# Performance work log

Measured on AMD Instinct MI355X. Metric: run time of the kernel, lower is better.

## Reference

```python
import jax, jax.numpy as jnp
import numpy as np

B, T, F = 8, 8192, 512
FREQ = T // 2 + 1


def setup_inputs() -> dict:
    key = jax.random.key(0)
    k1, k2 = jax.random.split(key)
    x = jax.random.normal(k1, (B, T, F), dtype=jnp.float32)
    # learnable complex filter stored as [F, FREQ, 2] (real, imag)
    H = jax.random.normal(k2, (F, FREQ, 2), dtype=jnp.float32) * 0.1
    # identity-ish init like the module: real part centered at 1
    H = H.at[..., 0].add(1.0)
    return {"x": x, "H": H}


def reference(x, H):
    # X: [B, FREQ, F] complex
    X = jnp.fft.rfft(x, axis=1, norm="ortho")
    Hc = (H[..., 0] + 1j * H[..., 1]).T  # [FREQ, F]
    Y = X * Hc[None, :, :]
    y = jnp.fft.irfft(Y, n=T, axis=1, norm="ortho")  # [B, T, F] real
    return y
```

## Files before the change

kernel.cpp:

```cpp
#include <hip/hip_runtime.h>


#define THREADS 512
#define NFFT 8192
#define TT 8192
#define FFD2 256
#define FREQ 4097

#define IDX(i) ((i) + ((i) >> 5))
#define LDS_SZ (NFFT + NFFT / 32)

__device__ __forceinline__ float2 cmul(float2 a, float2 b) {
    return make_float2(a.x * b.x - a.y * b.y, a.x * b.y + a.y * b.x);
}

#define BF1(i0, i1) { float2 a = v[i0], b = v[i1]; \
    v[i0] = make_float2(a.x + b.x, a.y + b.y); \
    v[i1] = make_float2(a.x - b.x, a.y - b.y); }
#define BFI(i0, i1) { float2 a = v[i0], b = v[i1]; \
    v[i0] = make_float2(a.x + b.x, a.y + b.y); \
    float dr = a.x - b.x, di = a.y - b.y; \
    v[i1] = make_float2(-di * S, dr * S); }
#define BFW(i0, i1, wr, wi) { float2 a = v[i0], b = v[i1]; \
    v[i0] = make_float2(a.x + b.x, a.y + b.y); \
    float dr = a.x - b.x, di = a.y - b.y; \
    v[i1] = make_float2(dr * (wr) - di * (wi), dr * (wi) + di * (wr)); }

template<int SGN>
__device__ __forceinline__ void dft16(float2 v[16]) {
    constexpr float S  = (float)SGN;
    constexpr float RT = 0.70710678118654752440f;
    constexpr float C1 = 0.92387953251128675613f;
    constexpr float S1 = 0.38268343236508977173f;
    BF1(0, 8); BFW(1, 9, C1, S * S1); BFW(2, 10, RT, S * RT); BFW(3, 11, S1, S * C1);
    BFI(4, 12); BFW(5, 13, -S1, S * C1); BFW(6, 14, -RT, S * RT); BFW(7, 15, -C1, S * S1);
    BF1(0, 4); BFW(1, 5, RT, S * RT); BFI(2, 6); BFW(3, 7, -RT, S * RT);
    BF1(8, 12); BFW(9, 13, RT, S * RT); BFI(10, 14); BFW(11, 15, -RT, S * RT);
    BF1(0, 2); BFI(1, 3); BF1(4, 6); BFI(5, 7);
    BF1(8, 10); BFI(9, 11); BF1(12, 14); BFI(13, 15);
    BF1(0, 1); BF1(2, 3); BF1(4, 5); BF1(6, 7);
    BF1(8, 9); BF1(10, 11); BF1(12, 13); BF1(14, 15);
}

__global__ __launch_bounds__(THREADS, 4) void fft_filter_kernel(
    const float* __restrict__ x, const float* __restrict__ H,
    float* __restrict__ y)
{
    __shared__ float re[LDS_SZ];
    __shared__ float im[LDS_SZ];

    const int tid = threadIdx.x;
    const int wg = blockIdx.x;
    const int id = (wg & 7) * 256 + (wg >> 3);
    const int b  = id >> 8;
    const int j  = id & 255;

    const float2* __restrict__ xp = (const float2*)x;
    float2* __restrict__ yp = (float2*)y;
    const size_t base = (size_t)b * TT * FFD2 + j;

    constexpr int R4[16] = {0, 8, 4, 12, 2, 10, 6, 14, 1, 9, 5, 13, 3, 11, 7, 15};
    const float TWO_PI = 6.28318530717958647692f;

    float2 v[16];

    {
        const int r1 = tid;
#pragma unroll
        for (int t = 0; t < 16; ++t)
            v[t] = xp[base + (size_t)((t * 512 + r1) * FFD2)];
        dft16<-1>(v);
        float sn, cs;
        __sincosf(-TWO_PI * (float)r1 / 8192.0f, &sn, &cs);
        const float2 wb = make_float2(cs, sn);
        float2 w = make_float2(1.0f, 0.0f);
#pragma unroll
        for (int u = 0; u < 16; ++u) {
            const float2 val = (u == 0) ? v[0] : cmul(v[R4[u]], w);
            const int a = IDX(u * 512 + r1);
            re[a] = val.x; im[a] = val.y;
            w = cmul(w, wb);
        }
    }
    __syncthreads();

    {
        const int ub = tid >> 5, r2 = tid & 31;
        const int bb = ub * 512 + r2;
#pragma unroll
        for (int t = 0; t < 16; ++t) {
            const int a = IDX(bb + t * 32);
            v[t] = make_float2(re[a], im[a]);
        }
        dft16<-1>(v);
        float sn, cs;
        __sincosf(-TWO_PI * (float)r2 / 512.0f, &sn, &cs);
        const float2 wb = make_float2(cs, sn);
        float2 w = make_float2(1.0f, 0.0f);
#pragma unroll
        for (int u = 0; u < 16; ++u) {
            const float2 val = (u == 0) ? v[0] : cmul(v[R4[u]], w);
            const int a = IDX(bb + u * 32);
            re[a] = val.x; im[a] = val.y;
            w = cmul(w, wb);
        }
    }
    __syncthreads();

    {
        const int b3 = tid >> 1, r3 = tid & 1;
        const int bb = b3 * 32 + r3;
#pragma unroll
        for (int t = 0; t < 16; ++t) {
            const int a = IDX(bb + t * 2);
            v[t] = make_float2(re[a], im[a]);
        }
        dft16<-1>(v);
        float sn, cs;
        __sincosf(-TWO_PI * (float)r3 / 32.0f, &sn, &cs);
        const float2 wb = make_float2(cs, sn);
        float2 w = make_float2(1.0f, 0.0f);
#pragma unroll
        for (int u = 0; u < 16; ++u) {
            const float2 A = (u == 0) ? v[0] : cmul(v[R4[u]], w);
            float2 o;
            o.x = __shfl_xor(A.x, 1);
            o.y = __shfl_xor(A.y, 1);
            const float2 val = r3 ? make_float2(o.x - A.x, o.y - A.y)
                                  : make_float2(A.x + o.x, A.y + o.y);
            const int a = IDX(bb + u * 2);
            re[a] = val.x; im[a] = val.y;
            w = cmul(w, wb);
        }
    }
    __syncthreads();

    {
        const float2* __restrict__ Hp = (const float2*)H;
        const size_t hb0 = (size_t)(2 * j) * FREQ;
        const size_t hb1 = hb0 + FREQ;
        const float invN = 1.0f / 8192.0f;
#pragma unroll
        for (int q = 0; q < 16; ++q) {
            const int u = tid + q * THREADS;
            if (u == 0) {
                const int a = IDX(0);
                const float zr = re[a], zi = im[a];
                re[a] = zr * Hp[hb0].x * invN;
                im[a] = zi * Hp[hb1].x * invN;
            } else if (u == 1) {
                const int a = IDX(1);
                const float zr = re[a], zi = im[a];
                re[a] = zr * Hp[hb0 + 4096].x * invN;
                im[a] = zi * Hp[hb1 + 4096].x * invN;
            } else {
                const int k  = ((u >> 9) & 15) | (((u >> 5) & 15) << 4)
                             | (((u >> 1) & 15) << 8) | ((u & 1) << 12);
                const int k2 = NFFT - k;
                const int p2 = ((k2 & 15) << 9) | (((k2 >> 4) & 15) << 5)
                             | (((k2 >> 8) & 15) << 1) | ((k2 >> 12) & 1);
                if (u < p2) {
                    const bool swapd = (k > NFFT / 2);
                    const int klo = swapd ? k2 : k;
                    const int pz = swapd ? p2 : u;
                    const int pw = swapd ? u : p2;
                    const int az = IDX(pz), aw = IDX(pw);
                    const float z1r = re[az], z1i = im[az];
                    const float z2r = re[aw], z2i = im[aw];
                    const float xar = 0.5f * (z1r + z2r), xai = 0.5f * (z1i - z2i);
                    const float xbr = 0.5f * (z1i + z2i), xbi = 0.5f * (z2r - z1r);
                    const float2 ha  = Hp[hb0 + klo];
                    const float2 hbv = Hp[hb1 + klo];
                    const float har = ha.x * invN,  hai = ha.y * invN;
                    const float hbr = hbv.x * invN, hbi = hbv.y * invN;
                    const float yar = xar * har - xai * hai;
                    const float yai = xar * hai + xai * har;
                    const float ybr = xbr * hbr - xbi * hbi;
                    const float ybi = xbr * hbi + xbi * hbr;
                    re[az] = yar - ybi;
                    im[az] = yai + ybr;
                    re[aw] = yar + ybi;
                    im[aw] = ybr - yai;
                }
            }
        }
    }
    __syncthreads();

    {
        const int b3 = tid >> 1, r3 = tid & 1;
        const int bb = b3 * 32 + r3;
        float sn, cs;
        __sincosf(TWO_PI * (float)r3 / 32.0f, &sn, &cs);
        const float2 wb = make_float2(cs, sn);
        float2 w = make_float2(1.0f, 0.0f);
#pragma unroll
        for (int u = 0; u < 16; ++u) {
            const int a = IDX(bb + u * 2);
            const float2 o = make_float2(re[a], im[a]);
            float2 p;
            p.x = __shfl_xor(o.x, 1);
            p.y = __shfl_xor(o.y, 1);
            const float2 U = r3 ? make_float2(p.x - o.x, p.y - o.y)
                                : make_float2(o.x + p.x, o.y + p.y);
            v[u] = (u == 0) ? U : cmul(U, w);
            w = cmul(w, wb);
        }
        dft16<1>(v);
#pragma unroll
        for (int t = 0; t < 16; ++t) {
            const int a = IDX(bb + t * 2);
            re[a] = v[R4[t]].x; im[a] = v[R4[t]].y;
        }
    }
    __syncthreads();

    {
        const int ub = tid >> 5, r2 = tid & 31;
        const int bb = ub * 512 + r2;
        float sn, cs;
        __sincosf(TWO_PI * (float)r2 / 512.0f, &sn, &cs);
        const float2 wb = make_float2(cs, sn);
        float2 w = make_float2(1.0f, 0.0f);
#pragma unroll
        for (int u = 0; u < 16; ++u) {
            const int a = IDX(bb + u * 32);
            const float2 U = make_float2(re[a], im[a]);
            v[u] = (u == 0) ? U : cmul(U, w);
            w = cmul(w, wb);
        }
        dft16<1>(v);
#pragma unroll
        for (int t = 0; t < 16; ++t) {
            const int a = IDX(bb + t * 32);
            re[a] = v[R4[t]].x; im[a] = v[R4[t]].y;
        }
    }
    __syncthreads();

    {
        const int r1 = tid;
        float sn, cs;
        __sincosf(TWO_PI * (float)r1 / 8192.0f, &sn, &cs);
        const float2 wb = make_float2(cs, sn);
        float2 w = make_float2(1.0f, 0.0f);
#pragma unroll
        for (int u = 0; u < 16; ++u) {
            const int a = IDX(u * 512 + r1);
            const float2 U = make_float2(re[a], im[a]);
            v[u] = (u == 0) ? U : cmul(U, w);
            w = cmul(w, wb);
        }
        dft16<1>(v);
#pragma unroll
        for (int t = 0; t < 16; ++t)
            yp[base + (size_t)((t * 512 + r1) * FFD2)] = v[R4[t]];
    }
}

extern "C" void kernel_launch(void* const* d_in, const int* in_sizes, int n_in,
                              void* d_out, int out_size, void* d_ws, size_t ws_size,
                              hipStream_t stream) {
    const float* x = (const float*)d_in[0];
    const float* H = (const float*)d_in[1];
    float* y = (float*)d_out;
    fft_filter_kernel<<<dim3(2048), dim3(THREADS), 0, stream>>>(x, H, y);
}
```

Before: 419.3 us.

## Split fused FFT filter into three-kernel four-step FFT via workspace

Replaces the single fused kernel, where each workgroup ran a full 8192-point FFT in LDS, with three kernels. The first does a 64-point first-stage FFT with twiddles and writes to a global workspace. The second does 128-point FFTs plus the pointwise filter multiply, pairing conjugate-symmetric columns, and then the inverse 128-point stage. The third does the final inverse 64-point stage. The aim is to cut LDS use per block and raise occupancy and coalescing, at the cost of two extra full round trips of intermediate data through global memory.

```diff
diff --git a/kernel.cpp b/kernel.cpp
--- a/kernel.cpp
+++ b/kernel.cpp
@@ -1,14 +1,8 @@
 #include <hip/hip_runtime.h>
 
 
-#define THREADS 512
-#define NFFT 8192
-#define TT 8192
-#define FFD2 256
+#define TWO_PI 6.28318530717958647692f
 #define FREQ 4097
-
-#define IDX(i) ((i) + ((i) >> 5))
-#define LDS_SZ (NFFT + NFFT / 32)
 
 __device__ __forceinline__ float2 cmul(float2 a, float2 b) {
     return make_float2(a.x * b.x - a.y * b.y, a.x * b.y + a.y * b.x);
@@ -25,6 +19,15 @@
     v[i0] = make_float2(a.x + b.x, a.y + b.y); \
     float dr = a.x - b.x, di = a.y - b.y; \
     v[i1] = make_float2(dr * (wr) - di * (wi), dr * (wi) + di * (wr)); }
+
+template<int SGN>
+__device__ __forceinline__ void dft8(float2* v) {
+    constexpr float S  = (float)SGN;
+    constexpr float RT = 0.70710678118654752440f;
+    BF1(0, 4); BFW(1, 5, RT, S * RT); BFI(2, 6); BFW(3, 7, -RT, S * RT);
+    BF1(0, 2); BFI(1, 3); BF1(4, 6); BFI(5, 7);
+    BF1(0, 1); BF1(2, 3); BF1(4, 5); BF1(6, 7);
+}
 
 template<int SGN>
 __device__ __forceinline__ void dft16(float2 v[16]) {
@@ -42,227 +45,303 @@
     BF1(8, 9); BF1(10, 11); BF1(12, 13); BF1(14, 15);
 }
 
-__global__ __launch_bounds__(THREADS, 4) void fft_filter_kernel(
-    const float* __restrict__ x, const float* __restrict__ H,
-    float* __restrict__ y)
+__global__ __launch_bounds__(512, 4) void k_fwd64(
+    const float2* __restrict__ xp, float2* __restrict__ ws)
 {
-    __shared__ float re[LDS_SZ];
-    __shared__ float im[LDS_SZ];
-
+    __shared__ float2 lds[4096];
+    constexpr int R3[8] = {0, 4, 2, 6, 1, 5, 3, 7};
+    const int bid = blockIdx.x;
+    const int jt = bid & 3;
+    const int t2 = (bid >> 2) & 127;
+    const int b  = bid >> 9;
     const int tid = threadIdx.x;
-    const int wg = blockIdx.x;
-    const int id = (wg & 7) * 256 + (wg >> 3);
-    const int b  = id >> 8;
-    const int j  = id & 255;
-
-    const float2* __restrict__ xp = (const float2*)x;
-    float2* __restrict__ yp = (float2*)y;
-    const size_t base = (size_t)b * TT * FFD2 + j;
-
+    const int sub = tid >> 6;
+    const int jj  = tid & 63;
+    const int j   = jt * 64 + jj;
+
+    float2 v[8];
+    const size_t rowbase = ((size_t)b * 8192 + t2) * 256 + j;
+#pragma unroll
+    for (int ta = 0; ta < 8; ++ta)
+        v[ta] = xp[rowbase + (size_t)(8 * ta + sub) * (128 * 256)];
+    dft8<-1>(v);
+    {
+        float sn, cs; __sincosf(-TWO_PI * (float)sub / 64.0f, &sn, &cs);
+        const float2 step = make_float2(cs, sn);
+        float2 w = make_float2(1.f, 0.f);
+#pragma unroll
+        for (int ka = 0; ka < 8; ++ka) {
+            const float2 val = (ka == 0) ? v[0] : cmul(v[R3[ka]], w);
+            lds[(ka * 8 + sub) * 64 + jj] = val;
+            w = cmul(w, step);
+        }
+    }
+    __syncthreads();
+    float2 g[8];
+#pragma unroll
+    for (int tb = 0; tb < 8; ++tb) g[tb] = lds[(sub * 8 + tb) * 64 + jj];
+    dft8<-1>(g);
+    {
+        float sn, cs;
+        __sincosf(-TWO_PI * (float)(t2 * sub) / 8192.0f, &sn, &cs);
+        float2 w = make_float2(cs, sn);
+        __sincosf(-TWO_PI * (float)t2 / 1024.0f, &sn, &cs);
+        const float2 step = make_float2(cs, sn);
+        const size_t obase = ((size_t)b * 64 * 128 + t2) * 256 + j;
+#pragma unroll
+        for (int kb = 0; kb < 8; ++kb) {
+            const int k1 = sub + 8 * kb;
+            ws[obase + (size_t)k1 * (128 * 256)] = cmul(g[R3[kb]], w);
+            w = cmul(w, step);
+        }
+    }
+}
+
+__global__ __launch_bounds__(512, 2) void k_mid128(
+    float2* __restrict__ ws, const float2* __restrict__ Hp)
+{
+    __shared__ float2 Sm[64 * 133];
+    constexpr int R3[8] = {0, 4, 2, 6, 1, 5, 3, 7};
     constexpr int R4[16] = {0, 8, 4, 12, 2, 10, 6, 14, 1, 9, 5, 13, 3, 11, 7, 15};
-    const float TWO_PI = 6.28318530717958647692f;
-
-    float2 v[16];
-
-    {
-        const int r1 = tid;
-#pragma unroll
-        for (int t = 0; t < 16; ++t)
-            v[t] = xp[base + (size_t)((t * 512 + r1) * FFD2)];
+    const int bid = blockIdx.x;
+    const int jt = bid & 7;
+    const int c  = (bid >> 3) & 31;
+    const int b  = bid >> 8;
+    const int tid = threadIdx.x;
+    const int k1A = c;
+    const int k1B = (c == 0) ? 32 : 64 - c;
+    const int j0 = jt * 32;
+
+#pragma unroll
+    for (int m = 0; m < 16; ++m) {
+        const int e = tid + m * 512;
+        const int jj = e & 31;
+        const int t2 = (e >> 5) & 127;
+        const int ks = e >> 12;
+        const int k1 = ks ? k1B : k1A;
+        Sm[(ks * 32 + jj) * 133 + t2] =
+            ws[(((size_t)b * 64 + k1) * 128 + t2) * 256 + j0 + jj];
+    }
+    __syncthreads();
+
+    const int col = tid >> 3;
+    const int sub = tid & 7;
+    float2* Sc = &Sm[col * 133];
+
+    {
+        float2 v[16];
+#pragma unroll
+        for (int ta = 0; ta < 16; ++ta) v[ta] = Sc[8 * ta + sub];
         dft16<-1>(v);
+        float sn, cs; __sincosf(-TWO_PI * (float)sub / 128.0f, &sn, &cs);
+        const float2 step = make_float2(cs, sn);
+        float2 w = make_float2(1.f, 0.f);
+#pragma unroll
+        for (int ka = 0; ka < 16; ++ka) {
+            Sc[ka * 8 + sub] = (ka == 0) ? v[0] : cmul(v[R4[ka]], w);
+            w = cmul(w, step);
+        }
+    }
+    __syncthreads();
+
+    {
+        float2 v[8], u[8];
+#pragma unroll
+        for (int tb = 0; tb < 8; ++tb) v[tb] = Sc[sub * 8 + tb];
+#pragma unroll
+        for (int tb = 0; tb < 8; ++tb) u[tb] = Sc[(sub + 8) * 8 + tb];
+        dft8<-1>(v);
+        { float2* t = u; float2* v = t; dft8<-1>(v); }
+        __syncthreads();
+#pragma unroll
+        for (int kb = 0; kb < 8; ++kb) {
+            Sc[sub + 16 * kb]     = v[R3[kb]];
+            Sc[sub + 8 + 16 * kb] = u[R3[kb]];
+        }
+    }
+    __syncthreads();
+
+    const float invN = 1.0f / 8192.0f;
+    if (c != 0) {
+#pragma unroll
+        for (int m = 0; m < 8; ++m) {
+            const int i = tid + m * 512;
+            const int sel = i >> 11;
+            const int rem = i & 2047;
+            const int k2 = rem & 63;
+            const int jj = rem >> 6;
+            const int col_lo = sel ? (32 + jj) : jj;
+            const int col_hi = sel ? jj : (32 + jj);
+            const int klo = (sel ? k1B : k1A) + 64 * k2;
+            float2* Plo = &Sm[col_lo * 133 + k2];
+            float2* Phi = &Sm[col_hi * 133 + 127 - k2];
+            const int f0 = 2 * (j0 + jj);
+            const float2 z1 = *Plo, z2 = *Phi;
+            const float xar = 0.5f * (z1.x + z2.x), xai = 0.5f * (z1.y - z2.y);
+            const float xbr = 0.5f * (z1.y + z2.y), xbi = 0.5f * (z2.x - z1.x);
+            const float2 ha = Hp[(size_t)f0 * FREQ + klo];
+            const float2 hb = Hp[(size_t)(f0 + 1) * FREQ + klo];
+            const float har = ha.x * invN, hai = ha.y * invN;
+            const float hbr = hb.x * invN, hbi = hb.y * invN;
+            const float yar = xar * har - xai * hai, yai = xar * hai + xai * har;
+            const float ybr = xbr * hbr - xbi * hbi, ybi = xbr * hbi + xbi * hbr;
+            *Plo = make_float2(yar - ybi, yai + ybr);
+            *Phi = make_float2(yar + ybi, ybr - yai);
+        }
+    } else {
+        for (int m = 0; m < 9; ++m) {
+            const int i = tid + m * 512;
+            if (i >= 4128) break;
+            int colx, slo, shi, klo, jj;
+            bool special = false;
+            if (i < 2048) {
+                const int k2 = i & 63; jj = i >> 6;
+                colx = 32 + jj; slo = k2; shi = 127 - k2; klo = 32 + 64 * k2;
+            } else {
+                const int i2 = i - 2048;
+                jj = i2 / 65;
+                const int r = i2 - jj * 65;
+                colx = jj;
+                if (r == 0)       { slo = 0;  shi = 0;  klo = 0;    special = true; }
+                else if (r == 64) { slo = 64; shi = 64; klo = 4096; special = true; }
+                else              { slo = r; shi = 128 - r; klo = 64 * r; }
+            }
+            const int f0 = 2 * (j0 + jj);
+            float2* Plo = &Sm[colx * 133 + slo];
+            if (special) {
+                const float2 z = *Plo;
+                const float2 ha = Hp[(size_t)f0 * FREQ + klo];
+                const float2 hb = Hp[(size_t)(f0 + 1) * FREQ + klo];
+                *Plo = make_float2(z.x * ha.x * invN, z.y * hb.x * invN);
+            } else {
+                float2* Phi = &Sm[colx * 133 + shi];
+                const float2 z1 = *Plo, z2 = *Phi;
+                const float xar = 0.5f * (z1.x + z2.x), xai = 0.5f * (z1.y - z2.y);
+                const float xbr = 0.5f * (z1.y + z2.y), xbi = 0.5f * (z2.x - z1.x);
+                const float2 ha = Hp[(size_t)f0 * FREQ + klo];
+                const float2 hb = Hp[(size_t)(f0 + 1) * FREQ + klo];
+                const float har = ha.x * invN, hai = ha.y * invN;
+                const float hbr = hb.x * invN, hbi = hb.y * invN;
+                const float yar = xar * har - xai * hai, yai = xar * hai + xai * har;
+                const float ybr = xbr * hbr - xbi * hbi, ybi = xbr * hbi + xbi * hbr;
+                *Plo = make_float2(yar - ybi, yai + ybr);
+                *Phi = make_float2(yar + ybi, ybr - yai);
+            }
+        }
+    }
+    __syncthreads();
+
+    {
+        float2 v[8], u[8];
+#pragma unroll
+        for (int kb = 0; kb < 8; ++kb) v[kb] = Sc[sub + 16 * kb];
+#pragma unroll
+        for (int kb = 0; kb < 8; ++kb) u[kb] = Sc[sub + 8 + 16 * kb];
+        dft8<1>(v);
+        { float2* t = u; float2* v = t; dft8<1>(v); }
         float sn, cs;
-        __sincosf(-TWO_PI * (float)r1 / 8192.0f, &sn, &cs);
-        const float2 wb = make_float2(cs, sn);
-        float2 w = make_float2(1.0f, 0.0f);
-#pragma unroll
-        for (int u = 0; u < 16; ++u) {
-            const float2 val = (u == 0) ? v[0] : cmul(v[R4[u]], w);
-            const int a = IDX(u * 512 + r1);
-            re[a] = val.x; im[a] = val.y;
-            w = cmul(w, wb);
-        }
-    }
-    __syncthreads();
-
-    {
-        const int ub = tid >> 5, r2 = tid & 31;
-        const int bb = ub * 512 + r2;
-#pragma unroll
-        for (int t = 0; t < 16; ++t) {
-            const int a = IDX(bb + t * 32);
-            v[t] = make_float2(re[a], im[a]);
-        }
-        dft16<-1>(v);
+        __sincosf(TWO_PI * (float)sub / 128.0f, &sn, &cs);
+        const float2 st0 = make_float2(cs, sn);
+        __sincosf(TWO_PI * (float)(sub + 8) / 128.0f, &sn, &cs);
+        const float2 st1 = make_float2(cs, sn);
+        float2 w0 = make_float2(1.f, 0.f), w1 = make_float2(1.f, 0.f);
+        float2 o0[8], o1[8];
+#pragma unroll
+        for (int tb = 0; tb < 8; ++tb) {
+            o0[tb] = (tb == 0) ? v[0] : cmul(v[R3[tb]], w0);
+            o1[tb] = (tb == 0) ? u[0] : cmul(u[R3[tb]], w1);
+            w0 = cmul(w0, st0); w1 = cmul(w1, st1);
+        }
+        __syncthreads();
+#pragma unroll
+        for (int tb = 0; tb < 8; ++tb) {
+            Sc[sub * 8 + tb] = o0[tb];
+            Sc[(sub + 8) * 8 + tb] = o1[tb];
+        }
+    }
+    __syncthreads();
+
+    {
+        const int k1c = (col >= 32) ? k1B : k1A;
+        float2 v[16];
+#pragma unroll
+        for (int ka = 0; ka < 16; ++ka) v[ka] = Sc[ka * 8 + sub];
+        dft16<1>(v);
         float sn, cs;
-        __sincosf(-TWO_PI * (float)r2 / 512.0f, &sn, &cs);
-        const float2 wb = make_float2(cs, sn);
-        float2 w = make_float2(1.0f, 0.0f);
-#pragma unroll
-        for (int u = 0; u < 16; ++u) {
-            const float2 val = (u == 0) ? v[0] : cmul(v[R4[u]], w);
-            const int a = IDX(bb + u * 32);
-            re[a] = val.x; im[a] = val.y;
-            w = cmul(w, wb);
-        }
-    }
-    __syncthreads();
-
-    {
-        const int b3 = tid >> 1, r3 = tid & 1;
-        const int bb = b3 * 32 + r3;
-#pragma unroll
-        for (int t = 0; t < 16; ++t) {
-            const int a = IDX(bb + t * 2);
-            v[t] = make_float2(re[a], im[a]);
-        }
-        dft16<-1>(v);
-        float sn, cs;
-        __sincosf(-TWO_PI * (float)r3 / 32.0f, &sn, &cs);
-        const float2 wb = make_float2(cs, sn);
-        float2 w = make_float2(1.0f, 0.0f);
-#pragma unroll
-        for (int u = 0; u < 16; ++u) {
-            const float2 A = (u == 0) ? v[0] : cmul(v[R4[u]], w);
-            float2 o;
-            o.x = __shfl_xor(A.x, 1);
-            o.y = __shfl_xor(A.y, 1);
-            const float2 val = r3 ? make_float2(o.x - A.x, o.y - A.y)
-                                  : make_float2(A.x + o.x, A.y + o.y);
-            const int a = IDX(bb + u * 2);
-            re[a] = val.x; im[a] = val.y;
-            w = cmul(w, wb);
-        }
-    }
-    __syncthreads();
-
-    {
-        const float2* __restrict__ Hp = (const float2*)H;
-        const size_t hb0 = (size_t)(2 * j) * FREQ;
-        const size_t hb1 = hb0 + FREQ;
-        const float invN = 1.0f / 8192.0f;
-#pragma unroll
-        for (int q = 0; q < 16; ++q) {
-            const int u = tid + q * THREADS;
-            if (u == 0) {
-                const int a = IDX(0);
-                const float zr = re[a], zi = im[a];
-                re[a] = zr * Hp[hb0].x * invN;
-                im[a] = zi * Hp[hb1].x * invN;
-            } else if (u == 1) {
-                const int a = IDX(1);
-                const float zr = re[a], zi = im[a];
-                re[a] = zr * Hp[hb0 + 4096].x * invN;
-                im[a] = zi * Hp[hb1 + 4096].x * invN;
-            } else {
-                const int k  = ((u >> 9) & 15) | (((u >> 5) & 15) << 4)
-                             | (((u >> 1) & 15) << 8) | ((u & 1) << 12);
-                const int k2 = NFFT - k;
-                const int p2 = ((k2 & 15) << 9) | (((k2 >> 4) & 15) << 5)
-                             | (((k2 >> 8) & 15) << 1) | ((k2 >> 12) & 1);
-                if (u < p2) {
-                    const bool swapd = (k > NFFT / 2);
-                    const int klo = swapd ? k2 : k;
-                    const int pz = swapd ? p2 : u;
-                    const int pw = swapd ? u : p2;
-                    const int az = IDX(pz), aw = IDX(pw);
-                    const float z1r = re[az], z1i = im[az];
-                    const float z2r = re[aw], z2i = im[aw];
-                    const float xar = 0.5f * (z1r + z2r), xai = 0.5f * (z1i - z2i);
-                    const float xbr = 0.5f * (z1i + z2i), xbi = 0.5f * (z2r - z1r);
-                    const float2 ha  = Hp[hb0 + klo];
-                    const float2 hbv = Hp[hb1 + klo];
-                    const float har = ha.x * invN,  hai = ha.y * invN;
-                    const float hbr = hbv.x * invN, hbi = hbv.y * invN;
-                    const float yar = xar * har - xai * hai;
-                    const float yai = xar * hai + xai * har;
-                    const float ybr = xbr * hbr - xbi * hbi;
-                    const float ybi = xbr * hbi + xbi * hbr;
-                    re[az] = yar - ybi;
-                    im[az] = yai + ybr;
-                    re[aw] = yar + ybi;
-                    im[aw] = ybr - yai;
-                }
-            }
-        }
-    }
-    __syncthreads();
-
-    {
-        const int b3 = tid >> 1, r3 = tid & 1;
-        const int bb = b3 * 32 + r3;
-        float sn, cs;
-        __sincosf(TWO_PI * (float)r3 / 32.0f, &sn, &cs);
-        const float2 wb = make_float2(cs, sn);
-        float2 w = make_float2(1.0f, 0.0f);
-#pragma unroll
-        for (int u = 0; u < 16; ++u) {
-            const int a = IDX(bb + u * 2);
-            const float2 o = make_float2(re[a], im[a]);
-            float2 p;
-            p.x = __shfl_xor(o.x, 1);
-            p.y = __shfl_xor(o.y, 1);
-            const float2 U = r3 ? make_float2(p.x - o.x, p.y - o.y)
-                                : make_float2(o.x + p.x, o.y + p.y);
-            v[u] = (u == 0) ? U : cmul(U, w);
-            w = cmul(w, wb);
-        }
-        dft16<1>(v);
-#pragma unroll
-        for (int t = 0; t < 16; ++t) {
-            const int a = IDX(bb + t * 2);
-            re[a] = v[R4[t]].x; im[a] = v[R4[t]].y;
-        }
-    }
-    __syncthreads();
-
-    {
-        const int ub = tid >> 5, r2 = tid & 31;
-        const int bb = ub * 512 + r2;
-        float sn, cs;
-        __sincosf(TWO_PI * (float)r2 / 512.0f, &sn, &cs);
-        const float2 wb = make_float2(cs, sn);
-        float2 w = make_float2(1.0f, 0.0f);
-#pragma unroll
-        for (int u = 0; u < 16; ++u) {
-            const int a = IDX(bb + u * 32);
-            const float2 U = make_float2(re[a], im[a]);
-            v[u] = (u == 0) ? U : cmul(U, w);
-            w = cmul(w, wb);
-        }
-        dft16<1>(v);
-#pragma unroll
-        for (int t = 0; t < 16; ++t) {
-            const int a = IDX(bb + t * 32);
-            re[a] = v[R4[t]].x; im[a] = v[R4[t]].y;
-        }
-    }
-    __syncthreads();
-
-    {
-        const int r1 = tid;
-        float sn, cs;
-        __sincosf(TWO_PI * (float)r1 / 8192.0f, &sn, &cs);
-        const float2 wb = make_float2(cs, sn);
-        float2 w = make_float2(1.0f, 0.0f);
-#pragma unroll
-        for (int u = 0; u < 16; ++u) {
-            const int a = IDX(u * 512 + r1);
-            const float2 U = make_float2(re[a], im[a]);
-            v[u] = (u == 0) ? U : cmul(U, w);
-            w = cmul(w, wb);
-        }
-        dft16<1>(v);
-#pragma unroll
-        for (int t = 0; t < 16; ++t)
-            yp[base + (size_t)((t * 512 + r1) * FFD2)] = v[R4[t]];
-    }
+        __sincosf(TWO_PI * (float)(sub * k1c) / 8192.0f, &sn, &cs);
+        float2 w = make_float2(cs, sn);
+        __sincosf(TWO_PI * (float)k1c / 1024.0f, &sn, &cs);
+        const float2 step = make_float2(cs, sn);
+#pragma unroll
+        for (int ta = 0; ta < 16; ++ta) {
+            Sc[8 * ta + sub] = cmul(v[R4[ta]], w);
+            w = cmul(w, step);
+        }
+    }
+    __syncthreads();
+
+#pragma unroll
+    for (int m = 0; m < 16; ++m) {
+        const int e = tid + m * 512;
+        const int jj = e & 31;
+        const int t2 = (e >> 5) & 127;
+        const int ks = e >> 12;
+        const int k1 = ks ? k1B : k1A;
+        ws[(((size_t)b * 64 + k1) * 128 + t2) * 256 + j0 + jj] =
+            Sm[(ks * 32 + jj) * 133 + t2];
+    }
+}
+
+__global__ __launch_bounds__(512, 4) void k_inv64(
+    const float2* __restrict__ ws, float2* __restrict__ yp)
+{
+    __shared__ float2 lds[4096];
+    constexpr int R3[8] = {0, 4, 2, 6, 1, 5, 3, 7};
+    const int bid = blockIdx.x;
+    const int jt = bid & 3;
+    const int t2 = (bid >> 2) & 127;
+    const int b  = bid >> 9;
+    const int tid = threadIdx.x;
+    const int sub = tid >> 6;
+    const int jj  = tid & 63;
+    const int j   = jt * 64 + jj;
+
+    float2 v[8];
+    const size_t ibase = ((size_t)b * 64 * 128 + t2) * 256 + j;
+#pragma unroll
+    for (int ka = 0; ka < 8; ++ka)
+        v[ka] = ws[ibase + (size_t)(8 * ka + sub) * (128 * 256)];
+    dft8<1>(v);
+    {
+        float sn, cs; __sincosf(TWO_PI * (float)sub / 64.0f, &sn, &cs);
+        const float2 step = make_float2(cs, sn);
+        float2 w = make_float2(1.f, 0.f);
+#pragma unroll
+        for (int ta = 0; ta < 8; ++ta) {
+            const float2 val = (ta == 0) ? v[0] : cmul(v[R3[ta]], w);
+            lds[(ta * 8 + sub) * 64 + jj] = val;
+            w = cmul(w, step);
+        }
+    }
+    __syncthreads();
+    float2 g[8];
+#pragma unroll
+    for (int kb = 0; kb < 8; ++kb) g[kb] = lds[(sub * 8 + kb) * 64 + jj];
+    dft8<1>(g);
+    const size_t rowbase = ((size_t)b * 8192 + t2) * 256 + j;
+#pragma unroll
+    for (int tb = 0; tb < 8; ++tb)
+        yp[rowbase + (size_t)(sub + 8 * tb) * (128 * 256)] = g[R3[tb]];
 }
 
 extern "C" void kernel_launch(void* const* d_in, const int* in_sizes, int n_in,
                               void* d_out, int out_size, void* d_ws, size_t ws_size,
                               hipStream_t stream) {
-    const float* x = (const float*)d_in[0];
-    const float* H = (const float*)d_in[1];
-    float* y = (float*)d_out;
-    fft_filter_kernel<<<dim3(2048), dim3(THREADS), 0, stream>>>(x, H, y);
-}
+    const float2* xp = (const float2*)d_in[0];
+    const float2* Hp = (const float2*)d_in[1];
+    float2* yp = (float2*)d_out;
+    float2* ws = (float2*)d_ws;
+    k_fwd64 <<<dim3(4096), dim3(512), 0, stream>>>(xp, ws);
+    k_mid128<<<dim3(2048), dim3(512), 0, stream>>>(ws, Hp);
+    k_inv64 <<<dim3(4096), dim3(512), 0, stream>>>(ws, yp);
+}
```

Measured after the change: 421.8 us. About the same (+0.6%).
